# Performance work log

Hardware: AMD Instinct MI355X
Metric: run time of the kernel (lower is better)

## Reference

```python
import jax, jax.numpy as jnp
import numpy as np

FP8_MAX = 448.0  # float8_e4m3fn max
EPS = 1e-6


def _rms_norm(x, w):
    # x: [T, H], w: [H]
    var = jnp.mean(x * x, axis=-1, keepdims=True)
    return x * jax.lax.rsqrt(var + EPS) * w


def _fused_add_rms_norm(x, resid, w):
    r = x + resid
    return _rms_norm(r, w), r


def _fp8_linear(y, W):
    # dynamic per-token activation quant + per-tensor weight quant, fp8 e4m3
    s = jnp.maximum(jnp.max(jnp.abs(y), axis=-1, keepdims=True) / FP8_MAX, 1e-12)  # [T,1]
    qx = jnp.clip(y / s, -FP8_MAX, FP8_MAX).astype(jnp.float8_e4m3fn).astype(jnp.float32)
    ws = jnp.maximum(jnp.max(jnp.abs(W)) / FP8_MAX, 1e-12)  # scalar
    qw = jnp.clip(W / ws, -FP8_MAX, FP8_MAX).astype(jnp.float8_e4m3fn).astype(jnp.float32)
    # out = dequant(qx) @ dequant(qw).T = (qx @ qw.T) * s * ws ; W is [out, in]
    return (qx @ qw.T) * (s * ws)


def setup_inputs() -> dict:
    key = jax.random.key(0)
    ks = jax.random.split(key, 8)
    H, T = 4096, 4096
    x = jax.random.normal(ks[0], (T, H), dtype=jnp.float32)
    nw0 = 1.0 + 0.02 * jax.random.normal(ks[1], (H,), dtype=jnp.float32)
    nw1 = 1.0 + 0.02 * jax.random.normal(ks[2], (H,), dtype=jnp.float32)
    nw2 = 1.0 + 0.02 * jax.random.normal(ks[3], (H,), dtype=jnp.float32)
    nw3 = 1.0 + 0.02 * jax.random.normal(ks[4], (H,), dtype=jnp.float32)
    W0 = 0.02 * jax.random.normal(ks[5], (H, H), dtype=jnp.float32)
    W1 = 0.02 * jax.random.normal(ks[6], (H, H), dtype=jnp.float32)
    W2 = 0.02 * jax.random.normal(ks[7], (H, H), dtype=jnp.float32)
    return {"x": x, "nw0": nw0, "nw1": nw1, "nw2": nw2, "nw3": nw3,
            "W0": W0, "W1": W1, "W2": W2}


def reference(x, nw0, nw1, nw2, nw3, W0, W1, W2):
    x = jax.nn.relu(x)
    resid = x
    y = _rms_norm(x, nw0)
    x2 = _fp8_linear(y, W0)
    y2, resid = _fused_add_rms_norm(x2, resid, nw1)
    x3 = _fp8_linear(y2, W1)
    y3, resid = _fused_add_rms_norm(x3, resid, nw2)
    x4 = _fp8_linear(y3, W2)
    y4, resid = _fused_add_rms_norm(x4, resid, nw3)
    return y4
```

## Files before the change

kernel.cpp:

```cpp
#include <hip/hip_runtime.h>
#include <cstdint>
#include <cstddef>

#define AS1 __attribute__((address_space(1)))
#define AS3 __attribute__((address_space(3)))

typedef __attribute__((ext_vector_type(4))) float f32x4;
typedef __attribute__((ext_vector_type(16))) float f32x16;
typedef __attribute__((ext_vector_type(4))) int i32x4;
typedef __attribute__((ext_vector_type(8))) int i32x8;

constexpr int HD = 4096;
constexpr float FP8MAX = 448.0f;

__device__ inline uint32_t pack4_fp8(float a, float b, float c, float d) {
    int v = 0;
    v = __builtin_amdgcn_cvt_pk_fp8_f32(a, b, v, false);
    v = __builtin_amdgcn_cvt_pk_fp8_f32(c, d, v, true);
    return (uint32_t)v;
}

__device__ inline float clipmul(float y, float rcs) {
    float t = y * rcs;
    t = fminf(t, FP8MAX);
    t = fmaxf(t, -FP8MAX);
    return t;
}

__device__ inline uint32_t quant4(float4 v, float rcs) {
    return pack4_fp8(clipmul(v.x, rcs), clipmul(v.y, rcs),
                     clipmul(v.z, rcs), clipmul(v.w, rcs));
}

__global__ __launch_bounds__(256) void w_absmax(const float* __restrict__ W0,
                                                const float* __restrict__ W1,
                                                const float* __restrict__ W2,
                                                uint32_t* __restrict__ wmax) {
    __shared__ float red[4];
    const float* W = (blockIdx.z == 0) ? W0 : (blockIdx.z == 1 ? W1 : W2);
    const float4* W4 = (const float4*)W;
    const int n4 = HD * HD / 4;
    float m = 0.f;
    for (int i = blockIdx.x * blockDim.x + threadIdx.x; i < n4; i += gridDim.x * blockDim.x) {
        float4 v = W4[i];
        m = fmaxf(m, fmaxf(fmaxf(fabsf(v.x), fabsf(v.y)), fmaxf(fabsf(v.z), fabsf(v.w))));
    }
#pragma unroll
    for (int i = 32; i > 0; i >>= 1) m = fmaxf(m, __shfl_xor(m, i, 64));
    if ((threadIdx.x & 63) == 0) red[threadIdx.x >> 6] = m;
    __syncthreads();
    if (threadIdx.x == 0) {
        m = fmaxf(fmaxf(red[0], red[1]), fmaxf(red[2], red[3]));
        atomicMax((unsigned int*)(wmax + blockIdx.z), __float_as_uint(m));
    }
}

__global__ __launch_bounds__(256) void w_quant(const float* __restrict__ W,
                                               const uint32_t* __restrict__ wmaxbits,
                                               uint32_t* __restrict__ qw) {
    const float rsw = 1.0f / fmaxf(__uint_as_float(*wmaxbits) / FP8MAX, 1e-12f);
    const int i = blockIdx.x * blockDim.x + threadIdx.x;
    qw[i] = quant4(((const float4*)W)[i], rsw);
}

__global__ __launch_bounds__(256) void fused_rms(const float* __restrict__ xin,
                                                 const float* __restrict__ addin,
                                                 float* __restrict__ resid_out,
                                                 const float* __restrict__ nw,
                                                 uint32_t* __restrict__ qx,
                                                 float* __restrict__ srow,
                                                 float* __restrict__ yout,
                                                 const int mode,
                                                 const float* __restrict__ Wq,
                                                 const uint32_t* __restrict__ wqmaxbits,
                                                 uint32_t* __restrict__ qwout) {
    const int tid = threadIdx.x;
    if (blockIdx.x >= 4096) {
        const float rsw = 1.0f / fmaxf(__uint_as_float(*wqmaxbits) / FP8MAX, 1e-12f);
        const float4* W4 = (const float4*)Wq;
        int i = (blockIdx.x - 4096) * 256 + tid;
#pragma unroll
        for (int it = 0; it < 4; it++, i += 4096 * 256)
            qwout[i] = quant4(W4[i], rsw);
        return;
    }

    __shared__ float reds[4];
    __shared__ float redm[4];
    const int row = blockIdx.x;
    const size_t base = (size_t)row * HD;
    const float4* xr = (const float4*)(xin + base);
    const float4* nw4 = (const float4*)nw;

    float4 v[4], w[4];
    float ss = 0.f, pm = 0.f;
    if (mode == 0) {
#pragma unroll
        for (int j = 0; j < 4; j++) {
            float4 t = xr[tid + j * 256];
            w[j] = nw4[tid + j * 256];
            t.x = fmaxf(t.x, 0.f); t.y = fmaxf(t.y, 0.f);
            t.z = fmaxf(t.z, 0.f); t.w = fmaxf(t.w, 0.f);
            v[j] = t;
            ss += t.x * t.x + t.y * t.y + t.z * t.z + t.w * t.w;
            pm = fmaxf(pm, fmaxf(fmaxf(fabsf(t.x * w[j].x), fabsf(t.y * w[j].y)),
                                 fmaxf(fabsf(t.z * w[j].z), fabsf(t.w * w[j].w))));
        }
    } else {
        const float4* ar = (const float4*)(addin + base);
#pragma unroll
        for (int j = 0; j < 4; j++) {
            float4 t = xr[tid + j * 256];
            float4 a = ar[tid + j * 256];
            w[j] = nw4[tid + j * 256];
            t.x += a.x; t.y += a.y; t.z += a.z; t.w += a.w;
            v[j] = t;
            ss += t.x * t.x + t.y * t.y + t.z * t.z + t.w * t.w;
            pm = fmaxf(pm, fmaxf(fmaxf(fabsf(t.x * w[j].x), fabsf(t.y * w[j].y)),
                                 fmaxf(fabsf(t.z * w[j].z), fabsf(t.w * w[j].w))));
        }
    }
    if (resid_out) {
        float4* ro = (float4*)(resid_out + base);
#pragma unroll
        for (int j = 0; j < 4; j++) ro[tid + j * 256] = v[j];
    }

#pragma unroll
    for (int i = 32; i > 0; i >>= 1) {
        ss += __shfl_xor(ss, i, 64);
        pm = fmaxf(pm, __shfl_xor(pm, i, 64));
    }
    if ((tid & 63) == 0) { reds[tid >> 6] = ss; redm[tid >> 6] = pm; }
    __syncthreads();
    ss = (reds[0] + reds[1]) + (reds[2] + reds[3]);
    pm = fmaxf(fmaxf(redm[0], redm[1]), fmaxf(redm[2], redm[3]));

    const float rs = 1.0f / sqrtf(ss / (float)HD + 1e-6f);

    if (mode == 2) {
        float4* yo = (float4*)(yout + base);
#pragma unroll
        for (int j = 0; j < 4; j++) {
            float4 t;
            t.x = (v[j].x * rs) * w[j].x; t.y = (v[j].y * rs) * w[j].y;
            t.z = (v[j].z * rs) * w[j].z; t.w = (v[j].w * rs) * w[j].w;
            yo[tid + j * 256] = t;
        }
        return;
    }

    const float amax = pm * rs;
    const float s = fmaxf(amax / FP8MAX, 1e-12f);
    const float rcs = 1.0f / s;
    if (tid == 0) srow[row] = s;
    uint32_t* qr = qx + base / 4;
#pragma unroll
    for (int j = 0; j < 4; j++) {
        float4 t;
        t.x = (v[j].x * rs) * w[j].x; t.y = (v[j].y * rs) * w[j].y;
        t.z = (v[j].z * rs) * w[j].z; t.w = (v[j].w * rs) * w[j].w;
        qr[tid + j * 256] = quant4(t, rcs);
    }
}

__global__ __launch_bounds__(256) void gemm_fp8mx(const uint8_t* __restrict__ qx,
                                                  const uint8_t* __restrict__ qw,
                                                  const float* __restrict__ srow,
                                                  const uint32_t* __restrict__ wmaxbits,
                                                  float* __restrict__ out,
                                                  const float* __restrict__ Wnext,
                                                  const uint32_t* __restrict__ wnmaxbits,
                                                  uint32_t* __restrict__ qwnext) {
    __shared__ uint8_t As[128 * 128];
    __shared__ uint8_t Bs[128 * 128];

    const int tid = threadIdx.x;

    if (blockIdx.z == 1) {
        const float rsw = 1.0f / fmaxf(__uint_as_float(*wnmaxbits) / FP8MAX, 1e-12f);
        const float4* W4 = (const float4*)Wnext;
        int i = (blockIdx.y * 32 + blockIdx.x) * 256 + tid;
#pragma unroll
        for (int it = 0; it < 16; it++, i += 1024 * 256)
            qwnext[i] = quant4(W4[i], rsw);
        return;
    }

    const int wave = tid >> 6;
    const int lane = tid & 63;
    const int lr = lane & 31;
    const int lh = lane >> 5;

    const int m0 = blockIdx.y * 128;
    const int n0 = blockIdx.x * 128;
    const int wm = (wave >> 1) * 64;
    const int wn = (wave & 1) * 64;

    f32x16 acc[2][2];
#pragma unroll
    for (int i = 0; i < 2; i++)
#pragma unroll
        for (int j = 0; j < 2; j++)
#pragma unroll
            for (int e = 0; e < 16; e++) acc[i][j][e] = 0.f;

    const int strow = wave * 8 + (lane >> 3);
    const int sg = (lane & 7) ^ (lane >> 3);
    const uint8_t* aga = qx + (size_t)(m0 + strow) * HD + sg * 16;
    const uint8_t* bga = qw + (size_t)(n0 + strow) * HD + sg * 16;
    const int ldst = wave * 1024 + lane * 16;

    for (int k0 = 0; k0 < HD; k0 += 128) {
#pragma unroll
        for (int c = 0; c < 4; c++) {
            __builtin_amdgcn_global_load_lds((const AS1 void*)(aga + (size_t)c * 32 * HD + k0),
                                             (AS3 void*)(As + c * 4096 + ldst), 16, 0, 0);
            __builtin_amdgcn_global_load_lds((const AS1 void*)(bga + (size_t)c * 32 * HD + k0),
                                             (AS3 void*)(Bs + c * 4096 + ldst), 16, 0, 0);
        }
        __syncthreads();

#pragma unroll
        for (int kh = 0; kh < 2; kh++) {
            union { i32x8 v8; i32x4 v4[2]; } af[2], bf[2];
            const int kg0 = kh * 4 + lh * 2;
#pragma unroll
            for (int i = 0; i < 2; i++) {
                const int ar = wm + i * 32 + lr;
                const uint8_t* pa = As + ar * 128;
                af[i].v4[0] = *(const i32x4*)(pa + ((kg0 ^ (ar & 7)) << 4));
                af[i].v4[1] = *(const i32x4*)(pa + (((kg0 + 1) ^ (ar & 7)) << 4));
                const int br = wn + i * 32 + lr;
                const uint8_t* pb = Bs + br * 128;
                bf[i].v4[0] = *(const i32x4*)(pb + ((kg0 ^ (br & 7)) << 4));
                bf[i].v4[1] = *(const i32x4*)(pb + (((kg0 + 1) ^ (br & 7)) << 4));
            }
#pragma unroll
            for (int i = 0; i < 2; i++)
#pragma unroll
                for (int j = 0; j < 2; j++)
                    acc[i][j] = __builtin_amdgcn_mfma_scale_f32_32x32x64_f8f6f4(
                        af[i].v8, bf[j].v8, acc[i][j],
                        0, 0,
                        0, 0x7F7F7F7Fu,
                        0, 0x7F7F7F7Fu);
        }
        __syncthreads();
    }

    const float wsc = fmaxf(__uint_as_float(*wmaxbits) / FP8MAX, 1e-12f);
#pragma unroll
    for (int i = 0; i < 2; i++) {
#pragma unroll
        for (int reg = 0; reg < 16; reg++) {
            const int row = (reg & 3) + 8 * (reg >> 2) + 4 * lh;
            const int m = m0 + wm + i * 32 + row;
            const float sv = srow[m] * wsc;
            float* orow = out + (size_t)m * HD + n0 + wn + lr;
#pragma unroll
            for (int j = 0; j < 2; j++)
                orow[j * 32] = acc[i][j][reg] * sv;
        }
    }
}

extern "C" void kernel_launch(void* const* d_in, const int* in_sizes, int n_in,
                              void* d_out, int out_size, void* d_ws, size_t ws_size,
                              hipStream_t stream) {
    const float* x   = (const float*)d_in[0];
    const float* nw0 = (const float*)d_in[1];
    const float* nw1 = (const float*)d_in[2];
    const float* nw2 = (const float*)d_in[3];
    const float* nw3 = (const float*)d_in[4];
    const float* W0  = (const float*)d_in[5];
    const float* W1  = (const float*)d_in[6];
    const float* W2  = (const float*)d_in[7];
    float* out = (float*)d_out;

    char* ws = (char*)d_ws;
    const size_t MB = 1024 * 1024;
    float* x2 = out;

    const bool overlap = ws_size >= 118 * MB;

    if (overlap) {
        float*    resid = (float*)(ws);
        uint32_t* qx    = (uint32_t*)(ws + 64 * MB);
        uint32_t* qwA   = (uint32_t*)(ws + 80 * MB);
        uint32_t* qwB   = (uint32_t*)(ws + 96 * MB);
        float*    srow  = (float*)(ws + 112 * MB);
        uint32_t* wmax  = (uint32_t*)(ws + 112 * MB + 16384);

        hipMemsetAsync(wmax, 0, 12, stream);
        hipLaunchKernelGGL(w_absmax, dim3(1024, 1, 3), dim3(256), 0, stream, W0, W1, W2, wmax);

        hipLaunchKernelGGL(fused_rms, dim3(8192), dim3(256), 0, stream,
                           x, (const float*)nullptr, resid, nw0, qx, srow, (float*)nullptr, 0,
                           W0, wmax + 0, qwA);
        hipLaunchKernelGGL(gemm_fp8mx, dim3(32, 32, 2), dim3(256), 0, stream,
                           (const uint8_t*)qx, (const uint8_t*)qwA, srow, wmax + 0, x2,
                           W1, wmax + 1, qwB);
        hipLaunchKernelGGL(fused_rms, dim3(4096), dim3(256), 0, stream,
                           x2, (const float*)resid, resid, nw1, qx, srow, (float*)nullptr, 1,
                           (const float*)nullptr, (const uint32_t*)nullptr, (uint32_t*)nullptr);
        hipLaunchKernelGGL(gemm_fp8mx, dim3(32, 32, 2), dim3(256), 0, stream,
                           (const uint8_t*)qx, (const uint8_t*)qwB, srow, wmax + 1, x2,
                           W2, wmax + 2, qwA);
        hipLaunchKernelGGL(fused_rms, dim3(4096), dim3(256), 0, stream,
                           x2, (const float*)resid, resid, nw2, qx, srow, (float*)nullptr, 1,
                           (const float*)nullptr, (const uint32_t*)nullptr, (uint32_t*)nullptr);
        hipLaunchKernelGGL(gemm_fp8mx, dim3(32, 32, 1), dim3(256), 0, stream,
                           (const uint8_t*)qx, (const uint8_t*)qwA, srow, wmax + 2, x2,
                           (const float*)nullptr, (const uint32_t*)nullptr, (uint32_t*)nullptr);
        hipLaunchKernelGGL(fused_rms, dim3(4096), dim3(256), 0, stream,
                           x2, (const float*)resid, (float*)nullptr, nw3,
                           (uint32_t*)nullptr, (float*)nullptr, out, 2,
                           (const float*)nullptr, (const uint32_t*)nullptr, (uint32_t*)nullptr);
    } else {
        float*    resid = (float*)(ws);
        uint32_t* qx    = (uint32_t*)(ws + 64 * MB);
        uint32_t* qw    = (uint32_t*)(ws + 80 * MB);
        float*    srow  = (float*)(ws + 96 * MB);
        uint32_t* wmax  = (uint32_t*)(ws + 96 * MB + 16384);

        hipMemsetAsync(wmax, 0, 12, stream);
        hipLaunchKernelGGL(w_absmax, dim3(1024, 1, 3), dim3(256), 0, stream, W0, W1, W2, wmax);
        hipLaunchKernelGGL(fused_rms, dim3(4096), dim3(256), 0, stream,
                           x, (const float*)nullptr, resid, nw0, qx, srow, (float*)nullptr, 0,
                           (const float*)nullptr, (const uint32_t*)nullptr, (uint32_t*)nullptr);
        const float* Ws[3]  = {W0, W1, W2};
        const float* nws[3] = {nw1, nw2, nw3};
        for (int l = 0; l < 3; l++) {
            hipLaunchKernelGGL(w_quant, dim3(HD * HD / 4 / 256), dim3(256), 0, stream,
                               Ws[l], wmax + l, qw);
            hipLaunchKernelGGL(gemm_fp8mx, dim3(32, 32, 1), dim3(256), 0, stream,
                               (const uint8_t*)qx, (const uint8_t*)qw, srow, wmax + l, x2,
                               (const float*)nullptr, (const uint32_t*)nullptr, (uint32_t*)nullptr);
            if (l < 2) {
                hipLaunchKernelGGL(fused_rms, dim3(4096), dim3(256), 0, stream,
                                   x2, (const float*)resid, resid, nws[l], qx, srow,
                                   (float*)nullptr, 1,
                                   (const float*)nullptr, (const uint32_t*)nullptr, (uint32_t*)nullptr);
            } else {
                hipLaunchKernelGGL(fused_rms, dim3(4096), dim3(256), 0, stream,
                                   x2, (const float*)resid, (float*)nullptr, nws[l],
                                   (uint32_t*)nullptr, (float*)nullptr, out, 2,
                                   (const float*)nullptr, (const uint32_t*)nullptr, (uint32_t*)nullptr);
            }
        }
    }
}
```

Before: 647.7 us.

## Rewrite FP8 GEMM as 256x256 double-buffered pipeline, move weight quant into RMS kernel

The FP8 MFMA GEMM now uses 256x256 tiles with 512 threads (8 waves, 4x2 accumulators each), double-buffered LDS and a ping-pong schedule. It interleaves global_load_lds prefetch with MFMA bursts under s_setprio and explicit barriers and vmcnt waits. The next layer's weight quantization is moved out of the GEMM's extra z-slice and into the fused RMS kernel launches, which are widened to 8192 blocks. This aims to raise MFMA utilisation and hide load latency, at the cost of only 256 GEMM blocks, which can leave CUs underused, and of tight hand-written synchronisation.

```diff
diff --git a/kernel.cpp b/kernel.cpp
--- a/kernel.cpp
+++ b/kernel.cpp
@@ -164,94 +164,118 @@
     }
 }
 
-__global__ __launch_bounds__(256) void gemm_fp8mx(const uint8_t* __restrict__ qx,
-                                                  const uint8_t* __restrict__ qw,
-                                                  const float* __restrict__ srow,
-                                                  const uint32_t* __restrict__ wmaxbits,
-                                                  float* __restrict__ out,
-                                                  const float* __restrict__ Wnext,
-                                                  const uint32_t* __restrict__ wnmaxbits,
-                                                  uint32_t* __restrict__ qwnext) {
-    __shared__ uint8_t As[128 * 128];
-    __shared__ uint8_t Bs[128 * 128];
+typedef union { i32x8 v8; i32x4 v4[2]; } frag8;
+
+__global__ __launch_bounds__(512, 2) void gemm_fp8mx(const uint8_t* __restrict__ qx,
+                                                     const uint8_t* __restrict__ qw,
+                                                     const float* __restrict__ srow,
+                                                     const uint32_t* __restrict__ wmaxbits,
+                                                     float* __restrict__ out) {
+    __shared__ i32x4 AsL[2][2][1024];
+    __shared__ i32x4 BsL[2][2][1024];
 
     const int tid = threadIdx.x;
-
-    if (blockIdx.z == 1) {
-        const float rsw = 1.0f / fmaxf(__uint_as_float(*wnmaxbits) / FP8MAX, 1e-12f);
-        const float4* W4 = (const float4*)Wnext;
-        int i = (blockIdx.y * 32 + blockIdx.x) * 256 + tid;
-#pragma unroll
-        for (int it = 0; it < 16; it++, i += 1024 * 256)
-            qwnext[i] = quant4(W4[i], rsw);
-        return;
-    }
-
-    const int wave = tid >> 6;
-    const int lane = tid & 63;
-    const int lr = lane & 31;
-    const int lh = lane >> 5;
-
-    const int m0 = blockIdx.y * 128;
-    const int n0 = blockIdx.x * 128;
-    const int wm = (wave >> 1) * 64;
-    const int wn = (wave & 1) * 64;
-
-    f32x16 acc[2][2];
-#pragma unroll
-    for (int i = 0; i < 2; i++)
+    const int wave = tid >> 6, lane = tid & 63;
+    const int lr = lane & 31, lh = lane >> 5;
+    const int m0 = blockIdx.y * 256, n0 = blockIdx.x * 256;
+    const int wm = (wave >> 2) * 128, wn = (wave & 3) * 64;
+
+    const int str = tid >> 2;
+    const int skg = (tid & 3) ^ ((str >> 1) & 3);
+    const size_t srcA = (size_t)(m0 + str) * HD + (size_t)(skg * 16);
+    const size_t srcB = (size_t)(n0 + str) * HD + (size_t)(skg * 16);
+
+    f32x16 acc[4][2];
+#pragma unroll
+    for (int i = 0; i < 4; i++)
 #pragma unroll
         for (int j = 0; j < 2; j++)
 #pragma unroll
             for (int e = 0; e < 16; e++) acc[i][j][e] = 0.f;
 
-    const int strow = wave * 8 + (lane >> 3);
-    const int sg = (lane & 7) ^ (lane >> 3);
-    const uint8_t* aga = qx + (size_t)(m0 + strow) * HD + sg * 16;
-    const uint8_t* bga = qw + (size_t)(n0 + strow) * HD + sg * 16;
-    const int ldst = wave * 1024 + lane * 16;
-
-    for (int k0 = 0; k0 < HD; k0 += 128) {
-#pragma unroll
-        for (int c = 0; c < 4; c++) {
-            __builtin_amdgcn_global_load_lds((const AS1 void*)(aga + (size_t)c * 32 * HD + k0),
-                                             (AS3 void*)(As + c * 4096 + ldst), 16, 0, 0);
-            __builtin_amdgcn_global_load_lds((const AS1 void*)(bga + (size_t)c * 32 * HD + k0),
-                                             (AS3 void*)(Bs + c * 4096 + ldst), 16, 0, 0);
-        }
-        __syncthreads();
-
-#pragma unroll
-        for (int kh = 0; kh < 2; kh++) {
-            union { i32x8 v8; i32x4 v4[2]; } af[2], bf[2];
-            const int kg0 = kh * 4 + lh * 2;
-#pragma unroll
-            for (int i = 0; i < 2; i++) {
-                const int ar = wm + i * 32 + lr;
-                const uint8_t* pa = As + ar * 128;
-                af[i].v4[0] = *(const i32x4*)(pa + ((kg0 ^ (ar & 7)) << 4));
-                af[i].v4[1] = *(const i32x4*)(pa + (((kg0 + 1) ^ (ar & 7)) << 4));
-                const int br = wn + i * 32 + lr;
-                const uint8_t* pb = Bs + br * 128;
-                bf[i].v4[0] = *(const i32x4*)(pb + ((kg0 ^ (br & 7)) << 4));
-                bf[i].v4[1] = *(const i32x4*)(pb + (((kg0 + 1) ^ (br & 7)) << 4));
-            }
-#pragma unroll
-            for (int i = 0; i < 2; i++)
-#pragma unroll
-                for (int j = 0; j < 2; j++)
-                    acc[i][j] = __builtin_amdgcn_mfma_scale_f32_32x32x64_f8f6f4(
-                        af[i].v8, bf[j].v8, acc[i][j],
-                        0, 0,
-                        0, 0x7F7F7F7Fu,
-                        0, 0x7F7F7F7Fu);
-        }
-        __syncthreads();
+    frag8 af0, af1, af2, af3, bf0, bf1;
+
+#define STAGE_U(gp, soff, larr, koff) do {                                              \
+    __builtin_amdgcn_global_load_lds((const AS1 void*)((gp) + (soff) + (size_t)(koff)), \
+                                     (AS3 void*)((larr) + tid), 16, 0, 0);              \
+    __builtin_amdgcn_global_load_lds((const AS1 void*)((gp) + (soff) + (size_t)(koff) + 128u * HD), \
+                                     (AS3 void*)((larr) + 512 + tid), 16, 0, 0);        \
+} while (0)
+
+#define READ_F(dst, rbase, larr) do {                 \
+    const int r_ = (rbase);                           \
+    const i32x4* p_ = (larr) + r_ * 4;                \
+    const int sw_ = (r_ >> 1) & 3;                    \
+    dst.v4[0] = p_[(lh * 2) ^ sw_];                   \
+    dst.v4[1] = p_[(lh * 2 + 1) ^ sw_];               \
+} while (0)
+
+#define MFMA1(a_, b_, i_, j_)                                                            \
+    acc[i_][j_] = __builtin_amdgcn_mfma_scale_f32_32x32x64_f8f6f4(                       \
+        (a_).v8, (b_).v8, acc[i_][j_], 0, 0, 0, 0x7F7F7F7Fu, 0, 0x7F7F7F7Fu)
+
+#define MFMA4(a0_, a1_, r0_, r1_) do {               \
+    __builtin_amdgcn_s_setprio(1);                   \
+    MFMA1(a0_, bf0, r0_, 0);                         \
+    MFMA1(a0_, bf1, r0_, 1);                         \
+    MFMA1(a1_, bf0, r1_, 0);                         \
+    MFMA1(a1_, bf1, r1_, 1);                         \
+    __builtin_amdgcn_s_setprio(0);                   \
+} while (0)
+
+#define KTILE(bR, bS, knext) do {                                   \
+                       \
+    READ_F(af0, wm + lr,      &AsL[bR][0][0]);                      \
+    READ_F(af1, wm + 32 + lr, &AsL[bR][0][0]);                      \
+    READ_F(bf0, wn + lr,      &BsL[bR][0][0]);                      \
+    READ_F(bf1, wn + 32 + lr, &BsL[bR][0][0]);                      \
+    STAGE_U(qx, srcA, &AsL[bS][0][0], (knext));                     \
+    __builtin_amdgcn_s_barrier();                                   \
+    MFMA4(af0, af1, 0, 1);                                          \
+    __builtin_amdgcn_s_barrier();                                   \
+                     \
+    READ_F(af2, wm + 64 + lr, &AsL[bR][0][0]);                      \
+    READ_F(af3, wm + 96 + lr, &AsL[bR][0][0]);                      \
+    STAGE_U(qw, srcB, &BsL[bS][0][0], (knext));                     \
+    __builtin_amdgcn_s_barrier();                                   \
+    MFMA4(af2, af3, 2, 3);                                          \
+    asm volatile("s_waitcnt vmcnt(4)" ::: "memory");                \
+    __builtin_amdgcn_s_barrier();                                   \
+                       \
+    READ_F(af0, wm + lr,      &AsL[bR][1][0]);                      \
+    READ_F(af1, wm + 32 + lr, &AsL[bR][1][0]);                      \
+    READ_F(bf0, wn + lr,      &BsL[bR][1][0]);                      \
+    READ_F(bf1, wn + 32 + lr, &BsL[bR][1][0]);                      \
+    STAGE_U(qx, srcA, &AsL[bS][1][0], (knext) + 64);                \
+    __builtin_amdgcn_s_barrier();                                   \
+    MFMA4(af0, af1, 0, 1);                                          \
+    __builtin_amdgcn_s_barrier();                                   \
+                     \
+    READ_F(af2, wm + 64 + lr, &AsL[bR][1][0]);                      \
+    READ_F(af3, wm + 96 + lr, &AsL[bR][1][0]);                      \
+    STAGE_U(qw, srcB, &BsL[bS][1][0], (knext) + 64);                \
+    __builtin_amdgcn_s_barrier();                                   \
+    MFMA4(af2, af3, 2, 3);                                          \
+    asm volatile("s_waitcnt vmcnt(4)" ::: "memory");                \
+    __builtin_amdgcn_s_barrier();                                   \
+} while (0)
+
+    STAGE_U(qx, srcA, &AsL[0][0][0], 0);
+    STAGE_U(qw, srcB, &BsL[0][0][0], 0);
+    STAGE_U(qx, srcA, &AsL[0][1][0], 64);
+    STAGE_U(qw, srcB, &BsL[0][1][0], 64);
+    asm volatile("s_waitcnt vmcnt(4)" ::: "memory");
+    __builtin_amdgcn_s_barrier();
+
+#pragma unroll 1
+    for (int kt = 0; kt < 32; kt += 2) {
+        KTILE(0, 1, (kt + 1) * 128);
+        KTILE(1, 0, ((kt + 2) & 31) * 128);
     }
 
     const float wsc = fmaxf(__uint_as_float(*wmaxbits) / FP8MAX, 1e-12f);
 #pragma unroll
-    for (int i = 0; i < 2; i++) {
+    for (int i = 0; i < 4; i++) {
 #pragma unroll
         for (int reg = 0; reg < 16; reg++) {
             const int row = (reg & 3) + 8 * (reg >> 2) + 4 * lh;
@@ -263,6 +287,11 @@
                 orow[j * 32] = acc[i][j][reg] * sv;
         }
     }
+#undef KTILE
+#undef MFMA4
+#undef MFMA1
+#undef READ_F
+#undef STAGE_U
 }
 
 extern "C" void kernel_launch(void* const* d_in, const int* in_sizes, int n_in,
@@ -298,21 +327,18 @@
         hipLaunchKernelGGL(fused_rms, dim3(8192), dim3(256), 0, stream,
                            x, (const float*)nullptr, resid, nw0, qx, srow, (float*)nullptr, 0,
                            W0, wmax + 0, qwA);
-        hipLaunchKernelGGL(gemm_fp8mx, dim3(32, 32, 2), dim3(256), 0, stream,
-                           (const uint8_t*)qx, (const uint8_t*)qwA, srow, wmax + 0, x2,
+        hipLaunchKernelGGL(gemm_fp8mx, dim3(16, 16), dim3(512), 0, stream,
+                           (const uint8_t*)qx, (const uint8_t*)qwA, srow, wmax + 0, x2);
+        hipLaunchKernelGGL(fused_rms, dim3(8192), dim3(256), 0, stream,
+                           x2, (const float*)resid, resid, nw1, qx, srow, (float*)nullptr, 1,
                            W1, wmax + 1, qwB);
-        hipLaunchKernelGGL(fused_rms, dim3(4096), dim3(256), 0, stream,
-                           x2, (const float*)resid, resid, nw1, qx, srow, (float*)nullptr, 1,
-                           (const float*)nullptr, (const uint32_t*)nullptr, (uint32_t*)nullptr);
-        hipLaunchKernelGGL(gemm_fp8mx, dim3(32, 32, 2), dim3(256), 0, stream,
-                           (const uint8_t*)qx, (const uint8_t*)qwB, srow, wmax + 1, x2,
+        hipLaunchKernelGGL(gemm_fp8mx, dim3(16, 16), dim3(512), 0, stream,
+                           (const uint8_t*)qx, (const uint8_t*)qwB, srow, wmax + 1, x2);
+        hipLaunchKernelGGL(fused_rms, dim3(8192), dim3(256), 0, stream,
+                           x2, (const float*)resid, resid, nw2, qx, srow, (float*)nullptr, 1,
                            W2, wmax + 2, qwA);
-        hipLaunchKernelGGL(fused_rms, dim3(4096), dim3(256), 0, stream,
-                           x2, (const float*)resid, resid, nw2, qx, srow, (float*)nullptr, 1,
-                           (const float*)nullptr, (const uint32_t*)nullptr, (uint32_t*)nullptr);
-        hipLaunchKernelGGL(gemm_fp8mx, dim3(32, 32, 1), dim3(256), 0, stream,
-                           (const uint8_t*)qx, (const uint8_t*)qwA, srow, wmax + 2, x2,
-                           (const float*)nullptr, (const uint32_t*)nullptr, (uint32_t*)nullptr);
+        hipLaunchKernelGGL(gemm_fp8mx, dim3(16, 16), dim3(512), 0, stream,
+                           (const uint8_t*)qx, (const uint8_t*)qwA, srow, wmax + 2, x2);
         hipLaunchKernelGGL(fused_rms, dim3(4096), dim3(256), 0, stream,
                            x2, (const float*)resid, (float*)nullptr, nw3,
                            (uint32_t*)nullptr, (float*)nullptr, out, 2,
@@ -334,9 +360,8 @@
         for (int l = 0; l < 3; l++) {
             hipLaunchKernelGGL(w_quant, dim3(HD * HD / 4 / 256), dim3(256), 0, stream,
                                Ws[l], wmax + l, qw);
-            hipLaunchKernelGGL(gemm_fp8mx, dim3(32, 32, 1), dim3(256), 0, stream,
-                               (const uint8_t*)qx, (const uint8_t*)qw, srow, wmax + l, x2,
-                               (const float*)nullptr, (const uint32_t*)nullptr, (uint32_t*)nullptr);
+            hipLaunchKernelGGL(gemm_fp8mx, dim3(16, 16), dim3(512), 0, stream,
+                               (const uint8_t*)qx, (const uint8_t*)qw, srow, wmax + l, x2);
             if (l < 2) {
                 hipLaunchKernelGGL(fused_rms, dim3(4096), dim3(256), 0, stream,
                                    x2, (const float*)resid, resid, nws[l], qx, srow,
```

New measurement: 621.0 us. 4.1% less time.
